# Performance work log

Hardware: AMD Instinct MI355X
Metric: run time of the kernel (lower is better)

Reference implementation:

```python
import jax, jax.numpy as jnp
import numpy as np

B = 16          # number of point clouds in batch (points.batch.max()+1)
C = 256         # feature channels
N = 65536       # total points across batch
LIDAR_POINTS = 32768
NUM_UPSAMPLE_UNIT = 2
L = LIDAR_POINTS // (2 ** NUM_UPSAMPLE_UNIT)  # 8192, output length per sample


def setup_inputs() -> dict:
    key = jax.random.key(0)
    k1, k2, k3 = jax.random.split(key, 3)
    points_x = jax.random.normal(k1, (N, 3), dtype=jnp.float32)
    point_features = jax.random.normal(k2, (N, C), dtype=jnp.float32)
    # per-point batch id, sorted (torch_geometric convention)
    batch = jnp.sort(jax.random.randint(k3, (N,), 0, B)).astype(jnp.int32)
    return {"points_x": points_x, "point_features": point_features, "batch": batch}


def reference(points_x, point_features, batch):
    # Per-batch counts and start offsets (points are sorted by batch id).
    counts = jax.ops.segment_sum(jnp.ones((N,), jnp.int32), batch, num_segments=B)  # [B]
    offsets = jnp.concatenate([jnp.zeros((1,), jnp.int32), jnp.cumsum(counts)[:-1]])  # [B]
    # torch nn.Upsample(scale_factor=r, mode='nearest') with r = L/n maps
    # output index j -> input index floor(j / r) = floor(j * n / L).
    j = jnp.arange(L, dtype=jnp.int32)                      # [L]
    src = offsets[:, None] + (j[None, :] * counts[:, None]) // L  # [B, L] global gather indices
    out_feature = point_features[src].transpose(0, 2, 1)    # [B, C, L]
    out_point = points_x[src, :3].transpose(0, 2, 1)        # [B, 3, L]
    return (out_point, out_feature)
```

## Files before the change

### kernel.cpp

```cpp
#include <hip/hip_runtime.h>

#define NPTS     65536
#define BATCHES  16
#define CHANNELS 256
#define LOUT     8192
#define TJ       64
#define NTILES   (LOUT / TJ)
#define MAX_ROWS 38
#define STRIDE   257

__global__ __launch_bounds__(256, 4) void k_main(
    const float* __restrict__ px,
    const float* __restrict__ pf,
    const int*   __restrict__ batch,
    float*       __restrict__ out)
{
    __shared__ float tile[MAX_ROWS * STRIDE];
    __shared__ int   sb[2];

    const int t    = threadIdx.x;
    const int lane = t & 63;
    const int wv   = t >> 6;
    const int b    = blockIdx.x >> 7;
    const int j0   = (blockIdx.x & (NTILES - 1)) * TJ;

    if (t < 2) {
        const int target = b + t;
        int lo = 0;
        if (target >= BATCHES) {
            lo = NPTS;
        } else {
            int hi = NPTS;
            while (lo < hi) {
                const int mid = (lo + hi) >> 1;
                if (batch[mid] < target) lo = mid + 1; else hi = mid;
            }
        }
        sb[t] = lo;
    }
    __syncthreads();
    const int offs = sb[0];
    const int cnt  = sb[1] - sb[0];

    auto srow = [&](int j) -> int {
        const int s = offs + ((j * cnt) >> 13);
        return s < (NPTS - 1) ? s : (NPTS - 1);
    };

    const int s0 = srow(j0);
    const int s1 = srow(j0 + TJ - 1);
    const int R  = s1 - s0 + 1;

    const int j  = j0 + lane;
    const int ga = srow(j);

    float* outf = out + (size_t)BATCHES * 3 * LOUT;

    if (R <= MAX_ROWS) {
        const float4* in4 = (const float4*)(pf + (size_t)s0 * CHANNELS);
        const int n4 = R * (CHANNELS / 4);
        for (int e = t; e < n4; e += 256) {
            const int row = e >> 6;
            const int c4  = e & 63;
            const float4 v = in4[row * 64 + c4];
            float* dst = &tile[row * STRIDE + c4 * 4];
            dst[0] = v.x; dst[1] = v.y; dst[2] = v.z; dst[3] = v.w;
        }
        __syncthreads();

        const int la = (ga - s0) * STRIDE;
        float* op = outf + ((size_t)b * CHANNELS) * LOUT + j;
        #pragma unroll 8
        for (int c = wv; c < CHANNELS; c += 4) {
            __builtin_nontemporal_store(tile[la + c], op + (size_t)c * LOUT);
        }
    } else {
        const float* ra = pf + (size_t)ga * CHANNELS;
        float* op = outf + ((size_t)b * CHANNELS) * LOUT + j;
        for (int c = wv; c < CHANNELS; c += 4) {
            __builtin_nontemporal_store(ra[c], op + (size_t)c * LOUT);
        }
    }

    if (wv < 3) {
        __builtin_nontemporal_store(px[ga * 3 + wv],
                                    out + ((size_t)(b * 3 + wv)) * LOUT + j);
    }
}

extern "C" void kernel_launch(void* const* d_in, const int* in_sizes, int n_in,
                              void* d_out, int out_size, void* d_ws, size_t ws_size,
                              hipStream_t stream) {
    const float* px    = (const float*)d_in[0];
    const float* pf    = (const float*)d_in[1];
    const int*   batch = (const int*)d_in[2];
    float* out = (float*)d_out;

    k_main<<<BATCHES * NTILES, 256, 0, stream>>>(px, pf, batch, out);
}
```

Baseline: 200.5 us.

## Retile gather over channel groups and wider j tiles with 8-byte stores

Splits channels into four groups of 64 and widens each block's output tile from 64 to 256 positions, so the grid becomes batch × channel-group × j-tile with the same total block count. Each lane now writes two adjacent output positions as an 8-byte nontemporal store, aiming for wider, more coalesced writes. The shared tile is narrowed to 64 channels so more source rows fit. It adds redundant binary searches per channel group and more complex LDS indexing.

```diff
diff --git a/kernel.cpp b/kernel.cpp
--- a/kernel.cpp
+++ b/kernel.cpp
@@ -4,10 +4,14 @@
 #define BATCHES  16
 #define CHANNELS 256
 #define LOUT     8192
-#define TJ       64
+#define TJ       256
+#define CGRP     64
 #define NTILES   (LOUT / TJ)
-#define MAX_ROWS 38
-#define STRIDE   257
+#define NCG      (CHANNELS / CGRP)
+#define MAX_ROWS 152
+#define STRIDE   (CGRP + 1)
+
+typedef float f32x2 __attribute__((ext_vector_type(2)));
 
 __global__ __launch_bounds__(256, 4) void k_main(
     const float* __restrict__ px,
@@ -21,8 +25,10 @@
     const int t    = threadIdx.x;
     const int lane = t & 63;
     const int wv   = t >> 6;
+    const int jt   = blockIdx.x & (NTILES - 1);
+    const int cg   = (blockIdx.x >> 5) & (NCG - 1);
     const int b    = blockIdx.x >> 7;
-    const int j0   = (blockIdx.x & (NTILES - 1)) * TJ;
+    const int j0   = jt * TJ;
 
     if (t < 2) {
         const int target = b + t;
@@ -51,40 +57,63 @@
     const int s1 = srow(j0 + TJ - 1);
     const int R  = s1 - s0 + 1;
 
-    const int j  = j0 + lane;
-    const int ga = srow(j);
+    int gA[2], gB[2];
+    #pragma unroll
+    for (int k = 0; k < 2; ++k) {
+        const int j = j0 + 2 * lane + 128 * k;
+        gA[k] = srow(j);
+        gB[k] = srow(j + 1);
+    }
 
     float* outf = out + (size_t)BATCHES * 3 * LOUT;
+    float* opBase = outf + ((size_t)(b * CHANNELS + cg * CGRP)) * LOUT + j0 + 2 * lane;
 
     if (R <= MAX_ROWS) {
-        const float4* in4 = (const float4*)(pf + (size_t)s0 * CHANNELS);
-        const int n4 = R * (CHANNELS / 4);
+        const float4* in4 = (const float4*)(pf + (size_t)s0 * CHANNELS + cg * CGRP);
+        const int n4 = R * (CGRP / 4);
         for (int e = t; e < n4; e += 256) {
-            const int row = e >> 6;
-            const int c4  = e & 63;
-            const float4 v = in4[row * 64 + c4];
+            const int row = e >> 4;
+            const int c4  = e & 15;
+            const float4 v = in4[row * (CHANNELS / 4) + c4];
             float* dst = &tile[row * STRIDE + c4 * 4];
             dst[0] = v.x; dst[1] = v.y; dst[2] = v.z; dst[3] = v.w;
         }
         __syncthreads();
 
-        const int la = (ga - s0) * STRIDE;
-        float* op = outf + ((size_t)b * CHANNELS) * LOUT + j;
-        #pragma unroll 8
-        for (int c = wv; c < CHANNELS; c += 4) {
-            __builtin_nontemporal_store(tile[la + c], op + (size_t)c * LOUT);
+        const int laA0 = (gA[0] - s0) * STRIDE, laB0 = (gB[0] - s0) * STRIDE;
+        const int laA1 = (gA[1] - s0) * STRIDE, laB1 = (gB[1] - s0) * STRIDE;
+        #pragma unroll 4
+        for (int c = wv; c < CGRP; c += 4) {
+            float* op = opBase + (size_t)c * LOUT;
+            f32x2 v0, v1;
+            v0.x = tile[laA0 + c]; v0.y = tile[laB0 + c];
+            v1.x = tile[laA1 + c]; v1.y = tile[laB1 + c];
+            __builtin_nontemporal_store(v0, (f32x2*)op);
+            __builtin_nontemporal_store(v1, (f32x2*)(op + 128));
         }
     } else {
-        const float* ra = pf + (size_t)ga * CHANNELS;
-        float* op = outf + ((size_t)b * CHANNELS) * LOUT + j;
-        for (int c = wv; c < CHANNELS; c += 4) {
-            __builtin_nontemporal_store(ra[c], op + (size_t)c * LOUT);
+        for (int c = wv; c < CGRP; c += 4) {
+            float* op = opBase + (size_t)c * LOUT;
+            const int cc = cg * CGRP + c;
+            f32x2 v0, v1;
+            v0.x = pf[(size_t)gA[0] * CHANNELS + cc];
+            v0.y = pf[(size_t)gB[0] * CHANNELS + cc];
+            v1.x = pf[(size_t)gA[1] * CHANNELS + cc];
+            v1.y = pf[(size_t)gB[1] * CHANNELS + cc];
+            __builtin_nontemporal_store(v0, (f32x2*)op);
+            __builtin_nontemporal_store(v1, (f32x2*)(op + 128));
         }
     }
 
-    if (wv < 3) {
-        __builtin_nontemporal_store(px[ga * 3 + wv],
-                                    out + ((size_t)(b * 3 + wv)) * LOUT + j);
+    if (cg == 0 && wv < 3) {
+        #pragma unroll
+        for (int k = 0; k < 2; ++k) {
+            f32x2 v;
+            v.x = px[gA[k] * 3 + wv];
+            v.y = px[gB[k] * 3 + wv];
+            __builtin_nontemporal_store(
+                v, (f32x2*)(out + ((size_t)(b * 3 + wv)) * LOUT + j0 + 2 * lane + 128 * k));
+        }
     }
 }
 
@@ -96,5 +125,5 @@
     const int*   batch = (const int*)d_in[2];
     float* out = (float*)d_out;
 
-    k_main<<<BATCHES * NTILES, 256, 0, stream>>>(px, pf, batch, out);
+    k_main<<<BATCHES * NCG * NTILES, 256, 0, stream>>>(px, pf, batch, out);
 }
```

New measurement: 198.6 us. Within noise of the previous version (-0.9%).
